# Optimization experiments

Hardware: AMD Instinct MI355X
Metric: run time of the kernel (lower is better)

## Reference

```python
import jax, jax.numpy as jnp
import numpy as np

L, H, P = 32768, 512, 256


def setup_inputs() -> dict:
    key = jax.random.key(0)
    ks = jax.random.split(key, 9)
    sH = 1.0 / np.sqrt(H).astype(np.float32)
    sP = 1.0 / np.sqrt(P).astype(np.float32)
    return {
        "input_sequence": jax.random.normal(ks[0], (L, H), jnp.float32),
        "Lambda_re": jax.random.normal(ks[1], (P,), jnp.float32),
        "Lambda_im": jax.random.normal(ks[2], (P,), jnp.float32) * np.float32(np.pi),
        "B_re": jax.random.normal(ks[3], (P, H), jnp.float32) * sH,
        "B_im": jax.random.normal(ks[4], (P, H), jnp.float32) * sH,
        "C_re": jax.random.normal(ks[5], (H, P), jnp.float32) * sP,
        "C_im": jax.random.normal(ks[6], (H, P), jnp.float32) * sP,
        "D": jax.random.normal(ks[7], (H,), jnp.float32),
        "log_step": jax.random.normal(ks[8], (P,), jnp.float32) - 3.0,
    }


def reference(input_sequence, Lambda_re, Lambda_im, B_re, B_im, C_re, C_im, D, log_step):
    # clip_eigs=True: enforce left-half-plane eigenvalues
    Lambda = jnp.clip(Lambda_re, None, -1e-4) + 1j * Lambda_im          # (P,)
    B_tilde = B_re + 1j * B_im                                          # (P,H)
    C_tilde = C_re + 1j * C_im                                          # (H,P)
    step = jnp.exp(log_step)                                            # step_rescale = 1.0, (P,)

    # ZOH discretization
    Lambda_bar = jnp.exp(Lambda * step)                                 # (P,) complex64
    B_bar = ((Lambda_bar - 1.0) / Lambda)[:, None] * B_tilde            # (P,H) complex64

    # Bu_elements: (L,P) complex; equivalent to vmap(lambda u: B_bar @ u)
    Bu = input_sequence.astype(B_bar.dtype) @ B_bar.T                   # (L,P)
    Lambda_elems = jnp.broadcast_to(Lambda_bar, (input_sequence.shape[0], Lambda_bar.shape[0]))

    def binop(q_i, q_j):
        A_i, b_i = q_i
        A_j, b_j = q_j
        return A_j * A_i, A_j * b_i + b_j

    _, xs = jax.lax.associative_scan(binop, (Lambda_elems, Bu))         # xs: (L,P)

    # conj_sym=True: ys = 2 * Re(C_tilde @ x) per step
    ys = 2.0 * (xs @ C_tilde.T).real                                    # (L,H)
    return ys + D * input_sequence
```

## Files before the change

### kernel.cpp

```cpp
#include <hip/hip_runtime.h>
#include <cstdint>
#include <cstddef>

typedef __bf16 bf16x8 __attribute__((ext_vector_type(8)));
typedef float f32x4 __attribute__((ext_vector_type(4)));

#define L_SEQ 32768
#define H_DIM 512
#define P_DIM 256
#define NP2   512
#define CHUNK 32
#define NCHUNK 1024
#define NSUPER 32

__device__ __forceinline__ void gload_lds16(const void* g, void* l) {
    __builtin_amdgcn_global_load_lds(
        (const __attribute__((address_space(1))) void*)g,
        (__attribute__((address_space(3))) void*)l,
        16, 0, 0);
}

__global__ void prep_kernel(const float* __restrict__ Lre, const float* __restrict__ Lim,
                            const float* __restrict__ lstep, float* __restrict__ par) {
    int p = threadIdx.x;
    if (p >= P_DIM) return;
    float lr = fminf(Lre[p], -1e-4f);
    float li = Lim[p];
    float st = expf(lstep[p]);
    float ldr = lr * st;
    float ldi = li * st;
    float er = expf(ldr);
    float ar = er * cosf(ldi);
    float ai = er * sinf(ldi);
    float den = lr * lr + li * li;
    float mr = ar - 1.0f, mi = ai;
    float cr = (mr * lr + mi * li) / den;
    float ci = (mi * lr - mr * li) / den;
    float e32  = expf((float)CHUNK * ldr);
    float ph32 = (float)CHUNK * ldi;
    float pr = e32 * cosf(ph32);
    float pi = e32 * sinf(ph32);
    par[p] = ar;        par[256 + p] = ai;
    par[512 + p] = cr;  par[768 + p] = ci;
    par[1024 + p] = pr; par[1280 + p] = pi;
    par[1536 + p] = ldr; par[1792 + p] = ldi;
}

__global__ void build_B_kernel(const float* __restrict__ Bre, const float* __restrict__ Bim,
                               const float* __restrict__ par, __bf16* __restrict__ Bt) {
    int idx = blockIdx.x * blockDim.x + threadIdx.x;
    int p = idx >> 9;
    int h = idx & 511;
    float cr = par[512 + p], ci = par[768 + p];
    float br = Bre[idx], bi = Bim[idx];
    Bt[(size_t)p * NP2 + h]         = (__bf16)(cr * br - ci * bi);
    Bt[(size_t)(256 + p) * NP2 + h] = (__bf16)(cr * bi + ci * br);
}

__global__ void build_C_kernel(const float* __restrict__ Cre, const float* __restrict__ Cim,
                               __bf16* __restrict__ Ct) {
    int idx = blockIdx.x * blockDim.x + threadIdx.x;
    int h = idx >> 8;
    int q = idx & 255;
    Ct[(size_t)h * NP2 + q]       = (__bf16)( 2.0f * Cre[idx]);
    Ct[(size_t)h * NP2 + 256 + q] = (__bf16)(-2.0f * Cim[idx]);
}

__global__ void cast_u_kernel(const float4* __restrict__ in, bf16x8* __restrict__ out, int n8) {
    int i = blockIdx.x * blockDim.x + threadIdx.x;
    if (i >= n8) return;
    float4 a = in[2 * i], b = in[2 * i + 1];
    bf16x8 v;
    v[0] = (__bf16)a.x; v[1] = (__bf16)a.y; v[2] = (__bf16)a.z; v[3] = (__bf16)a.w;
    v[4] = (__bf16)b.x; v[5] = (__bf16)b.y; v[6] = (__bf16)b.z; v[7] = (__bf16)b.w;
    out[i] = v;
}

template<bool FUSE>
__global__ __launch_bounds__(256)
void gemm_bt_kernel(const __bf16* __restrict__ A, const __bf16* __restrict__ Bt,
                    void* __restrict__ CoutV, const float* __restrict__ Dvec,
                    const __bf16* __restrict__ Ubf) {
    const int K = NP2, N = NP2;
    __shared__ __align__(16) __bf16 As[2][128 * 64];
    __shared__ __align__(16) __bf16 Bs[128 * 64];
    const int t = threadIdx.x;
    const int l = t & 63;
    const int w = t >> 6;
    const int wr = w >> 1, wc = w & 1;
    const int b    = blockIdx.x;
    const int n_sw = (b & 7) * 128 + (b >> 3);
    const int row0 = (n_sw >> 2) * 128;
    const int col0 = (n_sw & 3) * 128;
    const int lr = l & 15;
    const int lk = (l >> 4) * 8;
    f32x4 acc[4][4] = {};

    auto STAGE_A = [&](int buf, int k0) {
#pragma unroll
        for (int i = 0; i < 4; ++i) {
            int off = i * 256 + t;
            int r  = off >> 3;
            int ce = ((off & 7) ^ (r & 7)) * 8;
            gload_lds16(A + (size_t)(row0 + r) * K + (k0 + ce), &As[buf][off * 8]);
        }
    };
    auto STAGE_B = [&](int k0) {
#pragma unroll
        for (int i = 0; i < 4; ++i) {
            int off = i * 256 + t;
            int r  = off >> 3;
            int ce = ((off & 7) ^ (r & 7)) * 8;
            gload_lds16(Bt + (size_t)(col0 + r) * K + (k0 + ce), &Bs[off * 8]);
        }
    };

    auto COMPUTE = [&](int buf) {
#pragma unroll
        for (int kk = 0; kk < 64; kk += 32) {
            bf16x8 a[4], b2[4];
            const int ls = (kk + lk) >> 3;
#pragma unroll
            for (int m = 0; m < 4; ++m) {
                int row = wr * 64 + m * 16 + lr;
                a[m] = *reinterpret_cast<const bf16x8*>(&As[buf][row * 64 + ((ls ^ (row & 7)) << 3)]);
            }
#pragma unroll
            for (int n = 0; n < 4; ++n) {
                int row = wc * 64 + n * 16 + lr;
                b2[n] = *reinterpret_cast<const bf16x8*>(&Bs[row * 64 + ((ls ^ (row & 7)) << 3)]);
            }
            __builtin_amdgcn_s_setprio(1);
#pragma unroll
            for (int m = 0; m < 4; ++m)
#pragma unroll
                for (int n = 0; n < 4; ++n)
                    acc[m][n] = __builtin_amdgcn_mfma_f32_16x16x32_bf16(a[m], b2[n], acc[m][n], 0, 0, 0);
            __builtin_amdgcn_s_setprio(0);
        }
    };

    STAGE_A(0, 0);
    int cur = 0;
#pragma unroll
    for (int k0 = 0; k0 < K; k0 += 64) {
        STAGE_B(k0);
        if (k0 + 64 < K) {
            STAGE_A(cur ^ 1, k0 + 64);
            asm volatile("s_waitcnt vmcnt(4)" ::: "memory");
        } else {
            asm volatile("s_waitcnt vmcnt(0)" ::: "memory");
        }
        __builtin_amdgcn_s_barrier();
        __builtin_amdgcn_sched_barrier(0);
        COMPUTE(cur);
        __builtin_amdgcn_sched_barrier(0);
        __builtin_amdgcn_s_barrier();
        cur ^= 1;
    }

    const int lg = (l >> 4) * 4;
#pragma unroll
    for (int m = 0; m < 4; ++m) {
#pragma unroll
        for (int n = 0; n < 4; ++n) {
            int col = col0 + wc * 64 + n * 16 + lr;
#pragma unroll
            for (int j = 0; j < 4; ++j) {
                int row = row0 + wr * 64 + m * 16 + lg + j;
                size_t o = (size_t)row * N + col;
                if (FUSE) {
                    ((float*)CoutV)[o] = acc[m][n][j] + Dvec[col] * (float)Ubf[o];
                } else {
                    ((__bf16*)CoutV)[o] = (__bf16)acc[m][n][j];
                }
            }
        }
    }
}

__global__ void scanA_kernel(const __bf16* __restrict__ Bu, const float* __restrict__ par,
                             float* __restrict__ Fr, float* __restrict__ Fi) {
    int g = blockIdx.x;
    int p = threadIdx.x;
    float ar = par[p], ai = par[256 + p];
    const __bf16* bu = Bu + (size_t)g * CHUNK * NP2;
    float xr = 0.f, xi = 0.f;
#pragma unroll 4
    for (int i = 0; i < CHUNK; ++i) {
        float br = (float)bu[i * NP2 + p];
        float bi = (float)bu[i * NP2 + 256 + p];
        float nr = fmaf(ar, xr, fmaf(-ai, xi, br));
        float ni = fmaf(ar, xi, fmaf( ai, xr, bi));
        xr = nr; xi = ni;
    }
    Fr[g * 256 + p] = xr;
    Fi[g * 256 + p] = xi;
}

__global__ void scanB1_kernel(const float* __restrict__ Fr, const float* __restrict__ Fi,
                              const float* __restrict__ par,
                              float* __restrict__ Lr, float* __restrict__ Li,
                              float* __restrict__ Tr, float* __restrict__ Ti) {
    int s = blockIdx.x;
    int p = threadIdx.x;
    float pr = par[1024 + p], pi = par[1280 + p];
    float er = 0.f, ei = 0.f;
    int base = s * 32;
#pragma unroll
    for (int j = 0; j < 32; ++j) {
        int g = base + j;
        Lr[g * 256 + p] = er;
        Li[g * 256 + p] = ei;
        float fr = Fr[g * 256 + p], fi = Fi[g * 256 + p];
        float nr = fmaf(pr, er, fmaf(-pi, ei, fr));
        float ni = fmaf(pr, ei, fmaf( pi, er, fi));
        er = nr; ei = ni;
    }
    Tr[s * 256 + p] = er;
    Ti[s * 256 + p] = ei;
}

__global__ void scanB2_kernel(const float* __restrict__ Tr, const float* __restrict__ Ti,
                              const float* __restrict__ par,
                              float* __restrict__ Er, float* __restrict__ Ei) {
    int p = threadIdx.x;
    float ldr = par[1536 + p], ldi = par[1792 + p];
    float e  = expf(1024.0f * ldr);
    float ph = 1024.0f * ldi;
    float qr = e * cosf(ph), qi = e * sinf(ph);
    float er = 0.f, ei = 0.f;
#pragma unroll
    for (int s = 0; s < NSUPER; ++s) {
        Er[s * 256 + p] = er;
        Ei[s * 256 + p] = ei;
        float fr = Tr[s * 256 + p], fi = Ti[s * 256 + p];
        float nr = fmaf(qr, er, fmaf(-qi, ei, fr));
        float ni = fmaf(qr, ei, fmaf( qi, er, fi));
        er = nr; ei = ni;
    }
}

__global__ void scanC_kernel(const __bf16* __restrict__ Bu, const float* __restrict__ par,
                             const float* __restrict__ Lr, const float* __restrict__ Li,
                             const float* __restrict__ Er, const float* __restrict__ Ei,
                             __bf16* __restrict__ xs) {
    int g = blockIdx.x;
    int p = threadIdx.x;
    int s = g >> 5, k = g & 31;
    float ar = par[p], ai = par[256 + p];
    float ldr = par[1536 + p], ldi = par[1792 + p];
    float kk = (float)(32 * k);
    float e  = expf(kk * ldr);
    float ph = kk * ldi;
    float qr = e * cosf(ph), qi = e * sinf(ph);
    float er = Er[s * 256 + p], ei = Ei[s * 256 + p];
    float lr0 = Lr[g * 256 + p], li0 = Li[g * 256 + p];
    float xr = fmaf(qr, er, fmaf(-qi, ei, lr0));
    float xi = fmaf(qr, ei, fmaf( qi, er, li0));
    const __bf16* bu = Bu + (size_t)g * CHUNK * NP2;
    __bf16* xo = xs + (size_t)g * CHUNK * NP2;
#pragma unroll 4
    for (int i = 0; i < CHUNK; ++i) {
        float br = (float)bu[i * NP2 + p];
        float bi = (float)bu[i * NP2 + 256 + p];
        float nr = fmaf(ar, xr, fmaf(-ai, xi, br));
        float ni = fmaf(ar, xi, fmaf( ai, xr, bi));
        xr = nr; xi = ni;
        xo[i * NP2 + p]       = (__bf16)xr;
        xo[i * NP2 + 256 + p] = (__bf16)xi;
    }
}

extern "C" void kernel_launch(void* const* d_in, const int* in_sizes, int n_in,
                              void* d_out, int out_size, void* d_ws, size_t ws_size,
                              hipStream_t stream) {
    const float* u   = (const float*)d_in[0];
    const float* Lre = (const float*)d_in[1];
    const float* Lim = (const float*)d_in[2];
    const float* Bre = (const float*)d_in[3];
    const float* Bim = (const float*)d_in[4];
    const float* Cre = (const float*)d_in[5];
    const float* Cim = (const float*)d_in[6];
    const float* Dv  = (const float*)d_in[7];
    const float* lst = (const float*)d_in[8];

    char* w = (char*)d_ws;
    size_t off = 0;
    float* par = (float*)(w + off);      off += 16 * 1024;
    __bf16* Btm = (__bf16*)(w + off);    off += (size_t)NP2 * NP2 * 2;
    __bf16* Ctm = (__bf16*)(w + off);    off += (size_t)NP2 * NP2 * 2;
    float* Fr  = (float*)(w + off);      off += (size_t)NCHUNK * 256 * 4;
    float* Fi  = (float*)(w + off);      off += (size_t)NCHUNK * 256 * 4;
    float* Lr  = (float*)(w + off);      off += (size_t)NCHUNK * 256 * 4;
    float* Li  = (float*)(w + off);      off += (size_t)NCHUNK * 256 * 4;
    float* Tr  = (float*)(w + off);      off += (size_t)NSUPER * 256 * 4;
    float* Ti  = (float*)(w + off);      off += (size_t)NSUPER * 256 * 4;
    float* Er  = (float*)(w + off);      off += (size_t)NSUPER * 256 * 4;
    float* Ei  = (float*)(w + off);      off += (size_t)NSUPER * 256 * 4;
    __bf16* Ubf = (__bf16*)(w + off);    off += (size_t)L_SEQ * H_DIM * 2;
    __bf16* Xs  = (__bf16*)(w + off);    off += (size_t)L_SEQ * NP2 * 2;
    if (ws_size < off) return;

    __bf16* Bu = (__bf16*)d_out;

    prep_kernel   <<<1,    256, 0, stream>>>(Lre, Lim, lst, par);
    build_B_kernel<<<512,  256, 0, stream>>>(Bre, Bim, par, Btm);
    build_C_kernel<<<512,  256, 0, stream>>>(Cre, Cim, Ctm);
    cast_u_kernel <<<8192, 256, 0, stream>>>((const float4*)u, (bf16x8*)Ubf, L_SEQ * H_DIM / 8);
    gemm_bt_kernel<false><<<1024, 256, 0, stream>>>(Ubf, Btm, (void*)Bu, nullptr, nullptr);
    scanA_kernel  <<<NCHUNK, 256, 0, stream>>>(Bu, par, Fr, Fi);
    scanB1_kernel <<<NSUPER, 256, 0, stream>>>(Fr, Fi, par, Lr, Li, Tr, Ti);
    scanB2_kernel <<<1,      256, 0, stream>>>(Tr, Ti, par, Er, Ei);
    scanC_kernel  <<<NCHUNK, 256, 0, stream>>>(Bu, par, Lr, Li, Er, Ei, Xs);
    gemm_bt_kernel<true><<<1024, 256, 0, stream>>>(Xs, Ctm, d_out, Dv, Ubf);
}
```

Measured before the change: 104.1 us.

## Deepen GEMM LDS pipeline to triple-buffered A and double-buffered B; merge B/C builders

The GEMM main loop now keeps A in three LDS buffers and B in two, issuing loads two K-steps ahead for A and one ahead for B, with adjusted vmcnt waits. This lets global-to-LDS loads overlap compute more deeply instead of reloading B into a single buffer each step. LDS use grows from 48KB to 80KB per block, which may lower occupancy. Separately, the B and C weight-build kernels are merged into one launch to save a kernel launch.

```diff
diff --git a/kernel.cpp b/kernel.cpp
--- a/kernel.cpp
+++ b/kernel.cpp
@@ -46,24 +46,26 @@
     par[1536 + p] = ldr; par[1792 + p] = ldi;
 }
 
-__global__ void build_B_kernel(const float* __restrict__ Bre, const float* __restrict__ Bim,
-                               const float* __restrict__ par, __bf16* __restrict__ Bt) {
-    int idx = blockIdx.x * blockDim.x + threadIdx.x;
-    int p = idx >> 9;
-    int h = idx & 511;
-    float cr = par[512 + p], ci = par[768 + p];
-    float br = Bre[idx], bi = Bim[idx];
-    Bt[(size_t)p * NP2 + h]         = (__bf16)(cr * br - ci * bi);
-    Bt[(size_t)(256 + p) * NP2 + h] = (__bf16)(cr * bi + ci * br);
-}
-
-__global__ void build_C_kernel(const float* __restrict__ Cre, const float* __restrict__ Cim,
-                               __bf16* __restrict__ Ct) {
-    int idx = blockIdx.x * blockDim.x + threadIdx.x;
-    int h = idx >> 8;
-    int q = idx & 255;
-    Ct[(size_t)h * NP2 + q]       = (__bf16)( 2.0f * Cre[idx]);
-    Ct[(size_t)h * NP2 + 256 + q] = (__bf16)(-2.0f * Cim[idx]);
+__global__ void build_BC_kernel(const float* __restrict__ Bre, const float* __restrict__ Bim,
+                                const float* __restrict__ par,
+                                const float* __restrict__ Cre, const float* __restrict__ Cim,
+                                __bf16* __restrict__ Bt, __bf16* __restrict__ Ct) {
+    int b = blockIdx.x;
+    if (b < 512) {
+        int idx = b * 256 + threadIdx.x;
+        int p = idx >> 9;
+        float cr = par[512 + p], ci = par[768 + p];
+        float br = Bre[idx], bi = Bim[idx];
+        int h = idx & 511;
+        Bt[(size_t)p * NP2 + h]         = (__bf16)(cr * br - ci * bi);
+        Bt[(size_t)(256 + p) * NP2 + h] = (__bf16)(cr * bi + ci * br);
+    } else {
+        int idx = (b - 512) * 256 + threadIdx.x;
+        int h = idx >> 8;
+        int q = idx & 255;
+        Ct[(size_t)h * NP2 + q]       = (__bf16)( 2.0f * Cre[idx]);
+        Ct[(size_t)h * NP2 + 256 + q] = (__bf16)(-2.0f * Cim[idx]);
+    }
 }
 
 __global__ void cast_u_kernel(const float4* __restrict__ in, bf16x8* __restrict__ out, int n8) {
@@ -82,8 +84,8 @@
                     void* __restrict__ CoutV, const float* __restrict__ Dvec,
                     const __bf16* __restrict__ Ubf) {
     const int K = NP2, N = NP2;
-    __shared__ __align__(16) __bf16 As[2][128 * 64];
-    __shared__ __align__(16) __bf16 Bs[128 * 64];
+    __shared__ __align__(16) __bf16 As[3][128 * 64];
+    __shared__ __align__(16) __bf16 Bs[2][128 * 64];
     const int t = threadIdx.x;
     const int l = t & 63;
     const int w = t >> 6;
@@ -105,17 +107,17 @@
             gload_lds16(A + (size_t)(row0 + r) * K + (k0 + ce), &As[buf][off * 8]);
         }
     };
-    auto STAGE_B = [&](int k0) {
+    auto STAGE_B = [&](int buf, int k0) {
 #pragma unroll
         for (int i = 0; i < 4; ++i) {
             int off = i * 256 + t;
             int r  = off >> 3;
             int ce = ((off & 7) ^ (r & 7)) * 8;
-            gload_lds16(Bt + (size_t)(col0 + r) * K + (k0 + ce), &Bs[off * 8]);
+            gload_lds16(Bt + (size_t)(col0 + r) * K + (k0 + ce), &Bs[buf][off * 8]);
         }
     };
 
-    auto COMPUTE = [&](int buf) {
+    auto COMPUTE = [&](int ba, int bb) {
 #pragma unroll
         for (int kk = 0; kk < 64; kk += 32) {
             bf16x8 a[4], b2[4];
@@ -123,12 +125,12 @@
 #pragma unroll
             for (int m = 0; m < 4; ++m) {
                 int row = wr * 64 + m * 16 + lr;
-                a[m] = *reinterpret_cast<const bf16x8*>(&As[buf][row * 64 + ((ls ^ (row & 7)) << 3)]);
+                a[m] = *reinterpret_cast<const bf16x8*>(&As[ba][row * 64 + ((ls ^ (row & 7)) << 3)]);
             }
 #pragma unroll
             for (int n = 0; n < 4; ++n) {
                 int row = wc * 64 + n * 16 + lr;
-                b2[n] = *reinterpret_cast<const bf16x8*>(&Bs[row * 64 + ((ls ^ (row & 7)) << 3)]);
+                b2[n] = *reinterpret_cast<const bf16x8*>(&Bs[bb][row * 64 + ((ls ^ (row & 7)) << 3)]);
             }
             __builtin_amdgcn_s_setprio(1);
 #pragma unroll
@@ -141,22 +143,20 @@
     };
 
     STAGE_A(0, 0);
-    int cur = 0;
-#pragma unroll
-    for (int k0 = 0; k0 < K; k0 += 64) {
-        STAGE_B(k0);
-        if (k0 + 64 < K) {
-            STAGE_A(cur ^ 1, k0 + 64);
-            asm volatile("s_waitcnt vmcnt(4)" ::: "memory");
-        } else {
-            asm volatile("s_waitcnt vmcnt(0)" ::: "memory");
-        }
+    STAGE_B(0, 0);
+    STAGE_A(1, 64);
+#pragma unroll
+    for (int ks = 0; ks < 8; ++ks) {
+        if (ks + 1 < 8) STAGE_B((ks + 1) & 1, (ks + 1) * 64);
+        if (ks + 2 < 8) STAGE_A((ks + 2) % 3, (ks + 2) * 64);
+        if (ks <= 5)      { asm volatile("s_waitcnt vmcnt(12)" ::: "memory"); }
+        else if (ks == 6) { asm volatile("s_waitcnt vmcnt(8)"  ::: "memory"); }
+        else              { asm volatile("s_waitcnt vmcnt(0)"  ::: "memory"); }
         __builtin_amdgcn_s_barrier();
         __builtin_amdgcn_sched_barrier(0);
-        COMPUTE(cur);
+        COMPUTE(ks % 3, ks & 1);
         __builtin_amdgcn_sched_barrier(0);
         __builtin_amdgcn_s_barrier();
-        cur ^= 1;
     }
 
     const int lg = (l >> 4) * 4;
@@ -304,14 +304,13 @@
 
     __bf16* Bu = (__bf16*)d_out;
 
-    prep_kernel   <<<1,    256, 0, stream>>>(Lre, Lim, lst, par);
-    build_B_kernel<<<512,  256, 0, stream>>>(Bre, Bim, par, Btm);
-    build_C_kernel<<<512,  256, 0, stream>>>(Cre, Cim, Ctm);
-    cast_u_kernel <<<8192, 256, 0, stream>>>((const float4*)u, (bf16x8*)Ubf, L_SEQ * H_DIM / 8);
+    prep_kernel    <<<1,    256, 0, stream>>>(Lre, Lim, lst, par);
+    build_BC_kernel<<<1024, 256, 0, stream>>>(Bre, Bim, par, Cre, Cim, Btm, Ctm);
+    cast_u_kernel  <<<8192, 256, 0, stream>>>((const float4*)u, (bf16x8*)Ubf, L_SEQ * H_DIM / 8);
     gemm_bt_kernel<false><<<1024, 256, 0, stream>>>(Ubf, Btm, (void*)Bu, nullptr, nullptr);
-    scanA_kernel  <<<NCHUNK, 256, 0, stream>>>(Bu, par, Fr, Fi);
-    scanB1_kernel <<<NSUPER, 256, 0, stream>>>(Fr, Fi, par, Lr, Li, Tr, Ti);
-    scanB2_kernel <<<1,      256, 0, stream>>>(Tr, Ti, par, Er, Ei);
-    scanC_kernel  <<<NCHUNK, 256, 0, stream>>>(Bu, par, Lr, Li, Er, Ei, Xs);
+    scanA_kernel   <<<NCHUNK, 256, 0, stream>>>(Bu, par, Fr, Fi);
+    scanB1_kernel  <<<NSUPER, 256, 0, stream>>>(Fr, Fi, par, Lr, Li, Tr, Ti);
+    scanB2_kernel  <<<1,      256, 0, stream>>>(Tr, Ti, par, Er, Ei);
+    scanC_kernel   <<<NCHUNK, 256, 0, stream>>>(Bu, par, Lr, Li, Er, Ei, Xs);
     gemm_bt_kernel<true><<<1024, 256, 0, stream>>>(Xs, Ctm, d_out, Dv, Ubf);
 }
```

Measured after the change: 103.4 us. Within noise of the previous version (-0.7%).
